# Performance work log

Hardware: AMD Instinct MI355X
Metric: run time of the kernel (lower is better)

Reference implementation:

```python
import jax, jax.numpy as jnp
import numpy as np

T, B, IN_DIM = 1024, 8, 512
D_VALUE, D_KEY = 64, 64
V_TH = 1.0
EPS = 1e-08


def setup_inputs() -> dict:
    key = jax.random.key(0)
    ks = jax.random.split(key, 7)
    s_in = 1.0 / np.sqrt(IN_DIM)
    x = jax.random.normal(ks[0], (T, B, IN_DIM), dtype=jnp.float32)
    Wv = jax.random.uniform(ks[1], (D_VALUE, IN_DIM), jnp.float32, -s_in, s_in)
    bv = jax.random.uniform(ks[2], (D_VALUE,), jnp.float32, -s_in, s_in)
    Wk = jax.random.uniform(ks[3], (D_KEY, IN_DIM), jnp.float32, -s_in, s_in)
    bk = jax.random.uniform(ks[4], (D_KEY,), jnp.float32, -s_in, s_in)
    Wa = jax.random.uniform(ks[5], (D_KEY, IN_DIM), jnp.float32, -s_in, s_in)
    ba = jax.random.uniform(ks[6], (D_KEY,), jnp.float32, -s_in, s_in)
    return {"x": x, "Wv": Wv, "bv": bv, "Wk": Wk, "bk": bk, "Wa": Wa, "ba": ba}


def reference(x, Wv, bv, Wk, bk, Wa, ba):
    # projections: v (T,B,d), k (T,B,n), alpha (T,B,n)
    v = jnp.einsum('tbi,di->tbd', x, Wv) + bv
    k = jnp.einsum('tbi,ni->tbn', x, Wk) + bk
    alpha = jax.nn.sigmoid(jnp.einsum('tbi,ni->tbn', x, Wa) + ba)
    # outer-product writes: (T,B,d,n)
    writes = jnp.einsum('tbd,tbn->tbdn', v, k)
    # closed-form linear recurrence S_t = S_{t-1} * alpha_t + writes_t via cumprod/cumsum
    P = jnp.cumprod(alpha, axis=0)                       # (T,B,n)
    invP = 1.0 / (P + EPS)
    scaled = writes * invP[:, :, None, :]                # (T,B,d,n)
    S = jnp.cumsum(scaled, axis=0) * P[:, :, None, :]    # (T,B,d,n)
    Tt, Bb = x.shape[0], x.shape[1]
    mem = S.reshape(Tt, Bb, D_VALUE * D_KEY)
    spk = (mem > V_TH).astype(mem.dtype)
    return spk, mem
```

## Files before the change

kernel.cpp:

```cpp
#include <hip/hip_runtime.h>
#include <cmath>

#define TT 1024
#define BB 8
#define IND 512
#define NCH 32
#define CHL 32
#define EPSV 1e-8
#define OUTHALF ((size_t)TT * BB * 4096)

__global__ __launch_bounds__(256)
void k1_proj(const float* __restrict__ x,
             const float* __restrict__ Wv, const float* __restrict__ bv,
             const float* __restrict__ Wk, const float* __restrict__ bk,
             const float* __restrict__ Wa, const float* __restrict__ ba,
             float* __restrict__ vOut, float* __restrict__ kOut,
             double* __restrict__ aOut)
{
    __shared__ float sWt[64][192];
    __shared__ float sXt[64][32];
    const int tid = threadIdx.x;
    const int rowbase = blockIdx.x * 32;
    const int c0 = tid & 63;
    const int r0 = (tid >> 6) << 3;
    double av[8] = {}, ak[8] = {}, aa[8] = {};

    for (int ko = 0; ko < IND; ko += 64) {
        __syncthreads();
        if (tid < 192) {
            const float* src = (tid < 64  ? Wv + (size_t)tid * IND
                              : tid < 128 ? Wk + (size_t)(tid - 64) * IND
                              :             Wa + (size_t)(tid - 128) * IND) + ko;
            #pragma unroll
            for (int q = 0; q < 64; q += 4) {
                float4 w4 = *(const float4*)(src + q);
                sWt[q+0][tid] = w4.x; sWt[q+1][tid] = w4.y;
                sWt[q+2][tid] = w4.z; sWt[q+3][tid] = w4.w;
            }
        }
        {
            const int r  = tid & 31;
            const int kq = (tid >> 5) << 3;
            const float* xs = x + (size_t)(rowbase + r) * IND + ko + kq;
            float4 xa = *(const float4*)xs;
            float4 xb = *(const float4*)(xs + 4);
            sXt[kq+0][r] = xa.x; sXt[kq+1][r] = xa.y; sXt[kq+2][r] = xa.z; sXt[kq+3][r] = xa.w;
            sXt[kq+4][r] = xb.x; sXt[kq+5][r] = xb.y; sXt[kq+6][r] = xb.z; sXt[kq+7][r] = xb.w;
        }
        __syncthreads();

        float fv[8] = {}, fk[8] = {}, fa[8] = {};
        #pragma unroll
        for (int q = 0; q < 64; ++q) {
            float4 xa = *(const float4*)&sXt[q][r0];
            float4 xb = *(const float4*)&sXt[q][r0 + 4];
            float xr[8] = {xa.x, xa.y, xa.z, xa.w, xb.x, xb.y, xb.z, xb.w};
            float w0 = sWt[q][c0], w1 = sWt[q][c0 + 64], w2 = sWt[q][c0 + 128];
            #pragma unroll
            for (int j = 0; j < 8; ++j) {
                fv[j] = fmaf(xr[j], w0, fv[j]);
                fk[j] = fmaf(xr[j], w1, fk[j]);
                fa[j] = fmaf(xr[j], w2, fa[j]);
            }
        }
        #pragma unroll
        for (int j = 0; j < 8; ++j) { av[j] += fv[j]; ak[j] += fk[j]; aa[j] += fa[j]; }
    }

    #pragma unroll
    for (int j = 0; j < 8; ++j) {
        size_t r = (size_t)rowbase + r0 + j;
        vOut[r * 64 + c0] = (float)(av[j] + (double)bv[c0]);
        kOut[r * 64 + c0] = (float)(ak[j] + (double)bk[c0]);
        double z = aa[j] + (double)ba[c0];
        aOut[r * 64 + c0] = 1.0 / (1.0 + exp(-z));
    }
}

__global__ __launch_bounds__(256)
void k2a_chunkprod(const double* __restrict__ alpha, double* __restrict__ cpA)
{
    int gt = blockIdx.x * 256 + threadIdx.x;
    int ch = gt >> 9, chain = gt & 511;
    double p = 1.0;
    int base = (ch * CHL) * 512 + chain;
    for (int i = 0; i < CHL; ++i) p *= alpha[base + i * 512];
    cpA[gt] = p;
}

__global__ __launch_bounds__(256)
void kP_scan(const float* __restrict__ kIn, const double* __restrict__ alpha,
             const double* __restrict__ cpA,
             double* __restrict__ Parr, double* __restrict__ kdArr)
{
    int gt = blockIdx.x * 256 + threadIdx.x;
    int ch = gt >> 9, chain = gt & 511;
    double P = 1.0;
    for (int c = 0; c < ch; ++c) P *= cpA[c * 512 + chain];
    int base = (ch * CHL) * 512 + chain;
    for (int i = 0; i < CHL; ++i) {
        int idx = base + i * 512;
        P *= alpha[idx];
        Parr[idx] = P;
        kdArr[idx] = (double)kIn[idx] / (P + EPSV);
    }
}

__global__ __launch_bounds__(256)
void k3_csum(const float* __restrict__ vIn, const double* __restrict__ kdArr,
             double* __restrict__ Csum)
{
    __shared__ double sV[CHL * 64];
    const int tid = threadIdx.x;
    const int ch = blockIdx.x >> 3;
    const int b  = blockIdx.x & 7;
    #pragma unroll
    for (int q = 0; q < 8; ++q) {
        int idx = q * 256 + tid;
        int ti = idx >> 6, d = idx & 63;
        sV[idx] = (double)vIn[(((ch * CHL + ti) * BB) + b) * 64 + d];
    }
    __syncthreads();
    const int n = tid & 63;
    const int w = tid >> 6;
    double C[16];
    #pragma unroll
    for (int j = 0; j < 16; ++j) C[j] = 0.0;
    for (int i = 0; i < CHL; ++i) {
        double kd = kdArr[((ch * CHL + i) * BB + b) * 64 + n];
        const double* vrow = &sV[i * 64 + w * 16];
        #pragma unroll
        for (int j = 0; j < 16; ++j) C[j] = fma(vrow[j], kd, C[j]);
    }
    size_t cb = ((size_t)ch * 8 + b) * 4096 + (size_t)w * 1024 + n;
    #pragma unroll
    for (int j = 0; j < 16; ++j) Csum[cb + j * 64] = C[j];
}

__global__ __launch_bounds__(256)
void k3b_prefix(double* __restrict__ Csum)
{
    int s = blockIdx.x * 256 + threadIdx.x;
    int b = s >> 12, rest = s & 4095;
    double run = 0.0;
    for (int ch = 0; ch < NCH; ++ch) {
        size_t idx = ((size_t)ch * 8 + b) * 4096 + rest;
        double t = Csum[idx];
        Csum[idx] = run;
        run += t;
    }
}

__global__ __launch_bounds__(256)
void k4_scan(const float* __restrict__ vIn, const double* __restrict__ kdArr,
             const double* __restrict__ Parr, const double* __restrict__ Csum,
             float* __restrict__ outp)
{
    __shared__ double sV[CHL * 64];
    const int tid = threadIdx.x;
    const int ch = blockIdx.x >> 3;
    const int b  = blockIdx.x & 7;
    #pragma unroll
    for (int q = 0; q < 8; ++q) {
        int idx = q * 256 + tid;
        int ti = idx >> 6, d = idx & 63;
        sV[idx] = (double)vIn[(((ch * CHL + ti) * BB) + b) * 64 + d];
    }
    __syncthreads();
    const int n = tid & 63;
    const int w = tid >> 6;
    size_t cb = ((size_t)ch * 8 + b) * 4096 + (size_t)w * 1024 + n;
    double C[16];
    #pragma unroll
    for (int j = 0; j < 16; ++j) C[j] = Csum[cb + j * 64];

    float* spk = outp;
    float* mem = outp + OUTHALF;
    for (int i = 0; i < CHL; ++i) {
        int t = ch * CHL + i;
        int base = (t * BB + b) * 64 + n;
        double kd = kdArr[base];
        double P  = Parr[base];
        const double* vrow = &sV[i * 64 + w * 16];
        size_t ob = ((size_t)t * BB + b) * 4096 + (size_t)w * 1024 + n;
        #pragma unroll
        for (int j = 0; j < 16; ++j) {
            C[j] = fma(vrow[j], kd, C[j]);
            double S = P * C[j];
            mem[ob + j * 64] = (float)S;
            spk[ob + j * 64] = (S > 1.0) ? 1.0f : 0.0f;
        }
    }
}

extern "C" void kernel_launch(void* const* d_in, const int* in_sizes, int n_in,
                              void* d_out, int out_size, void* d_ws, size_t ws_size,
                              hipStream_t stream)
{
    const float* x  = (const float*)d_in[0];
    const float* Wv = (const float*)d_in[1];
    const float* bv = (const float*)d_in[2];
    const float* Wk = (const float*)d_in[3];
    const float* bk = (const float*)d_in[4];
    const float* Wa = (const float*)d_in[5];
    const float* ba = (const float*)d_in[6];
    float* out = (float*)d_out;

    char* ws = (char*)d_ws;
    float*  v     = (float*)(ws);
    float*  kk    = (float*)(ws + ( 2u << 20));
    double* alpha = (double*)(ws + ( 4u << 20));
    double* cpA   = (double*)(ws + ( 8u << 20));
    double* Parr  = (double*)(ws + ( 9u << 20));
    double* kdArr = (double*)(ws + (13u << 20));
    double* Csum  = (double*)(ws + (17u << 20));

    hipLaunchKernelGGL(k1_proj,       dim3(256), dim3(256), 0, stream,
                       x, Wv, bv, Wk, bk, Wa, ba, v, kk, alpha);
    hipLaunchKernelGGL(k2a_chunkprod, dim3(64),  dim3(256), 0, stream, alpha, cpA);
    hipLaunchKernelGGL(kP_scan,       dim3(64),  dim3(256), 0, stream,
                       kk, alpha, cpA, Parr, kdArr);
    hipLaunchKernelGGL(k3_csum,       dim3(256), dim3(256), 0, stream,
                       v, kdArr, Csum);
    hipLaunchKernelGGL(k3b_prefix,    dim3(128), dim3(256), 0, stream, Csum);
    hipLaunchKernelGGL(k4_scan,       dim3(256), dim3(256), 0, stream,
                       v, kdArr, Parr, Csum, out);
}
```

Baseline: 130.3 us.

## Fuse decay-product scan into chunk kernels, store alpha as float, split d across blocks

Stores alpha as float instead of double and removes the separate chunk-product and P/kd scan kernels. A single small kernel now computes exclusive per-chunk prefix products, and both the chunk-sum and output kernels recompute P and k/P locally from shared-memory alpha and k. Each (chunk, batch) is split across two blocks over the d dimension, doubling the grid, and the large output writes become nontemporal stores. This cuts workspace traffic and launches, but adds redundant divisions and puts a serial 8-block kernel on the critical path.

```diff
diff --git a/kernel.cpp b/kernel.cpp
--- a/kernel.cpp
+++ b/kernel.cpp
@@ -15,7 +15,7 @@
              const float* __restrict__ Wk, const float* __restrict__ bk,
              const float* __restrict__ Wa, const float* __restrict__ ba,
              float* __restrict__ vOut, float* __restrict__ kOut,
-             double* __restrict__ aOut)
+             float* __restrict__ aOut)
 {
     __shared__ float sWt[64][192];
     __shared__ float sXt[64][32];
@@ -73,68 +73,66 @@
         vOut[r * 64 + c0] = (float)(av[j] + (double)bv[c0]);
         kOut[r * 64 + c0] = (float)(ak[j] + (double)bk[c0]);
         double z = aa[j] + (double)ba[c0];
-        aOut[r * 64 + c0] = 1.0 / (1.0 + exp(-z));
-    }
-}
-
-__global__ __launch_bounds__(256)
-void k2a_chunkprod(const double* __restrict__ alpha, double* __restrict__ cpA)
-{
-    int gt = blockIdx.x * 256 + threadIdx.x;
-    int ch = gt >> 9, chain = gt & 511;
-    double p = 1.0;
-    int base = (ch * CHL) * 512 + chain;
-    for (int i = 0; i < CHL; ++i) p *= alpha[base + i * 512];
-    cpA[gt] = p;
-}
-
-__global__ __launch_bounds__(256)
-void kP_scan(const float* __restrict__ kIn, const double* __restrict__ alpha,
-             const double* __restrict__ cpA,
-             double* __restrict__ Parr, double* __restrict__ kdArr)
-{
-    int gt = blockIdx.x * 256 + threadIdx.x;
-    int ch = gt >> 9, chain = gt & 511;
-    double P = 1.0;
-    for (int c = 0; c < ch; ++c) P *= cpA[c * 512 + chain];
-    int base = (ch * CHL) * 512 + chain;
-    for (int i = 0; i < CHL; ++i) {
-        int idx = base + i * 512;
-        P *= alpha[idx];
-        Parr[idx] = P;
-        kdArr[idx] = (double)kIn[idx] / (P + EPSV);
-    }
-}
-
-__global__ __launch_bounds__(256)
-void k3_csum(const float* __restrict__ vIn, const double* __restrict__ kdArr,
+        aOut[r * 64 + c0] = (float)(1.0 / (1.0 + exp(-z)));
+    }
+}
+
+__global__ __launch_bounds__(64)
+void kPF(const float* __restrict__ alpha, double* __restrict__ cpA)
+{
+    int chain = blockIdx.x * 64 + threadIdx.x;
+    double run = 1.0;
+    for (int ch = 0; ch < NCH; ++ch) {
+        cpA[ch * 512 + chain] = run;
+        double p = 1.0;
+        #pragma unroll
+        for (int t = 0; t < CHL; ++t)
+            p *= (double)alpha[(ch * CHL + t) * 512 + chain];
+        run *= p;
+    }
+}
+
+__global__ __launch_bounds__(256)
+void k3_csum(const float* __restrict__ vIn, const float* __restrict__ kIn,
+             const float* __restrict__ alpha, const double* __restrict__ cpA,
              double* __restrict__ Csum)
 {
-    __shared__ double sV[CHL * 64];
+    __shared__ float  sA[CHL][64];
+    __shared__ float  sK[CHL][64];
+    __shared__ double sV[CHL][32];
     const int tid = threadIdx.x;
-    const int ch = blockIdx.x >> 3;
-    const int b  = blockIdx.x & 7;
+    const int ch = blockIdx.x >> 4;
+    const int b  = (blockIdx.x >> 1) & 7;
+    const int dh = blockIdx.x & 1;
     #pragma unroll
     for (int q = 0; q < 8; ++q) {
         int idx = q * 256 + tid;
-        int ti = idx >> 6, d = idx & 63;
-        sV[idx] = (double)vIn[(((ch * CHL + ti) * BB) + b) * 64 + d];
+        int t = idx >> 6, nn = idx & 63;
+        int g = ((ch * CHL + t) * BB + b) * 64 + nn;
+        sA[t][nn] = alpha[g];
+        sK[t][nn] = kIn[g];
+    }
+    #pragma unroll
+    for (int q = 0; q < 4; ++q) {
+        int idx = q * 256 + tid;
+        int t = idx >> 5, dd = idx & 31;
+        sV[t][dd] = (double)vIn[((ch * CHL + t) * BB + b) * 64 + dh * 32 + dd];
     }
     __syncthreads();
     const int n = tid & 63;
     const int w = tid >> 6;
-    double C[16];
-    #pragma unroll
-    for (int j = 0; j < 16; ++j) C[j] = 0.0;
-    for (int i = 0; i < CHL; ++i) {
-        double kd = kdArr[((ch * CHL + i) * BB + b) * 64 + n];
-        const double* vrow = &sV[i * 64 + w * 16];
-        #pragma unroll
-        for (int j = 0; j < 16; ++j) C[j] = fma(vrow[j], kd, C[j]);
-    }
-    size_t cb = ((size_t)ch * 8 + b) * 4096 + (size_t)w * 1024 + n;
-    #pragma unroll
-    for (int j = 0; j < 16; ++j) Csum[cb + j * 64] = C[j];
+    double P = cpA[ch * 512 + b * 64 + n];
+    double C[8] = {};
+    for (int t = 0; t < CHL; ++t) {
+        P *= (double)sA[t][n];
+        double kd = (double)sK[t][n] / (P + EPSV);
+        const double* vr = &sV[t][w * 8];
+        #pragma unroll
+        for (int j = 0; j < 8; ++j) C[j] = fma(vr[j], kd, C[j]);
+    }
+    size_t cb = ((size_t)ch * 8 + b) * 4096 + (size_t)(dh * 32 + w * 8) * 64 + n;
+    #pragma unroll
+    for (int j = 0; j < 8; ++j) Csum[cb + j * 64] = C[j];
 }
 
 __global__ __launch_bounds__(256)
@@ -152,43 +150,54 @@
 }
 
 __global__ __launch_bounds__(256)
-void k4_scan(const float* __restrict__ vIn, const double* __restrict__ kdArr,
-             const double* __restrict__ Parr, const double* __restrict__ Csum,
-             float* __restrict__ outp)
-{
-    __shared__ double sV[CHL * 64];
+void k4_scan(const float* __restrict__ vIn, const float* __restrict__ kIn,
+             const float* __restrict__ alpha, const double* __restrict__ cpA,
+             const double* __restrict__ Csum, float* __restrict__ outp)
+{
+    __shared__ float  sA[CHL][64];
+    __shared__ float  sK[CHL][64];
+    __shared__ double sV[CHL][32];
     const int tid = threadIdx.x;
-    const int ch = blockIdx.x >> 3;
-    const int b  = blockIdx.x & 7;
+    const int ch = blockIdx.x >> 4;
+    const int b  = (blockIdx.x >> 1) & 7;
+    const int dh = blockIdx.x & 1;
     #pragma unroll
     for (int q = 0; q < 8; ++q) {
         int idx = q * 256 + tid;
-        int ti = idx >> 6, d = idx & 63;
-        sV[idx] = (double)vIn[(((ch * CHL + ti) * BB) + b) * 64 + d];
+        int t = idx >> 6, nn = idx & 63;
+        int g = ((ch * CHL + t) * BB + b) * 64 + nn;
+        sA[t][nn] = alpha[g];
+        sK[t][nn] = kIn[g];
+    }
+    #pragma unroll
+    for (int q = 0; q < 4; ++q) {
+        int idx = q * 256 + tid;
+        int t = idx >> 5, dd = idx & 31;
+        sV[t][dd] = (double)vIn[((ch * CHL + t) * BB + b) * 64 + dh * 32 + dd];
     }
     __syncthreads();
     const int n = tid & 63;
     const int w = tid >> 6;
-    size_t cb = ((size_t)ch * 8 + b) * 4096 + (size_t)w * 1024 + n;
-    double C[16];
-    #pragma unroll
-    for (int j = 0; j < 16; ++j) C[j] = Csum[cb + j * 64];
+    double P = cpA[ch * 512 + b * 64 + n];
+    size_t cb = ((size_t)ch * 8 + b) * 4096 + (size_t)(dh * 32 + w * 8) * 64 + n;
+    double C[8];
+    #pragma unroll
+    for (int j = 0; j < 8; ++j) C[j] = Csum[cb + j * 64];
 
     float* spk = outp;
     float* mem = outp + OUTHALF;
-    for (int i = 0; i < CHL; ++i) {
-        int t = ch * CHL + i;
-        int base = (t * BB + b) * 64 + n;
-        double kd = kdArr[base];
-        double P  = Parr[base];
-        const double* vrow = &sV[i * 64 + w * 16];
-        size_t ob = ((size_t)t * BB + b) * 4096 + (size_t)w * 1024 + n;
-        #pragma unroll
-        for (int j = 0; j < 16; ++j) {
-            C[j] = fma(vrow[j], kd, C[j]);
+    for (int t = 0; t < CHL; ++t) {
+        P *= (double)sA[t][n];
+        double kd = (double)sK[t][n] / (P + EPSV);
+        const double* vr = &sV[t][w * 8];
+        size_t ob = ((size_t)((ch * CHL + t) * BB + b)) * 4096
+                  + (size_t)(dh * 32 + w * 8) * 64 + n;
+        #pragma unroll
+        for (int j = 0; j < 8; ++j) {
+            C[j] = fma(vr[j], kd, C[j]);
             double S = P * C[j];
-            mem[ob + j * 64] = (float)S;
-            spk[ob + j * 64] = (S > 1.0) ? 1.0f : 0.0f;
+            __builtin_nontemporal_store((float)S, &mem[ob + j * 64]);
+            __builtin_nontemporal_store((S > 1.0) ? 1.0f : 0.0f, &spk[ob + j * 64]);
         }
     }
 }
@@ -208,21 +217,17 @@
 
     char* ws = (char*)d_ws;
     float*  v     = (float*)(ws);
-    float*  kk    = (float*)(ws + ( 2u << 20));
-    double* alpha = (double*)(ws + ( 4u << 20));
-    double* cpA   = (double*)(ws + ( 8u << 20));
-    double* Parr  = (double*)(ws + ( 9u << 20));
-    double* kdArr = (double*)(ws + (13u << 20));
-    double* Csum  = (double*)(ws + (17u << 20));
-
-    hipLaunchKernelGGL(k1_proj,       dim3(256), dim3(256), 0, stream,
+    float*  kk    = (float*)(ws + (2u << 20));
+    float*  alpha = (float*)(ws + (4u << 20));
+    double* cpA   = (double*)(ws + (6u << 20));
+    double* Csum  = (double*)(ws + (7u << 20));
+
+    hipLaunchKernelGGL(k1_proj,    dim3(256), dim3(256), 0, stream,
                        x, Wv, bv, Wk, bk, Wa, ba, v, kk, alpha);
-    hipLaunchKernelGGL(k2a_chunkprod, dim3(64),  dim3(256), 0, stream, alpha, cpA);
-    hipLaunchKernelGGL(kP_scan,       dim3(64),  dim3(256), 0, stream,
-                       kk, alpha, cpA, Parr, kdArr);
-    hipLaunchKernelGGL(k3_csum,       dim3(256), dim3(256), 0, stream,
-                       v, kdArr, Csum);
-    hipLaunchKernelGGL(k3b_prefix,    dim3(128), dim3(256), 0, stream, Csum);
-    hipLaunchKernelGGL(k4_scan,       dim3(256), dim3(256), 0, stream,
-                       v, kdArr, Parr, Csum, out);
-}
+    hipLaunchKernelGGL(kPF,        dim3(8),   dim3(64),  0, stream, alpha, cpA);
+    hipLaunchKernelGGL(k3_csum,    dim3(512), dim3(256), 0, stream,
+                       v, kk, alpha, cpA, Csum);
+    hipLaunchKernelGGL(k3b_prefix, dim3(128), dim3(256), 0, stream, Csum);
+    hipLaunchKernelGGL(k4_scan,    dim3(512), dim3(256), 0, stream,
+                       v, kk, alpha, cpA, Csum, out);
+}
```

After: 142.7 us. 1.1x slower.
